# Kernel optimization log

Measured on AMD Instinct MI355X. Metric: run time of the kernel, lower is better.

## Reference

```python
import jax, jax.numpy as jnp
import numpy as np

N = 100000   # nodes
E = 1600000  # edges (avg degree 16)
IN = 128
HID = 128


def _glorot(key, shape):
    fan_in = shape[1]
    return jax.random.normal(key, shape, jnp.float32) * (1.0 / np.sqrt(fan_in))


def setup_inputs() -> dict:
    key = jax.random.key(0)
    ks = jax.random.split(key, 8)
    x = jax.random.normal(ks[0], (N, IN), jnp.float32)
    edge_index = jax.random.randint(ks[1], (2, E), 0, N, dtype=jnp.int64)
    return {
        "x": x,
        "edge_index": edge_index,
        "W1_l": _glorot(ks[2], (HID, IN)),
        "W1_r": _glorot(ks[3], (HID, IN)),
        "b1": jnp.zeros((HID,), jnp.float32),
        "W2_l": _glorot(ks[4], (HID, HID)),
        "W2_r": _glorot(ks[5], (HID, HID)),
        "b2": jnp.zeros((HID,), jnp.float32),
    }


def _sage_conv(x, src, dst, W_l, W_r, b):
    # message = x[src]; mean-aggregate onto dst; out = lin_l(mean) + lin_r(x) + b
    msg = x[src]                                                # [E, d]
    agg = jax.ops.segment_sum(msg, dst, num_segments=N)         # [N, d]
    cnt = jax.ops.segment_sum(jnp.ones((src.shape[0], 1), x.dtype), dst,
                              num_segments=N)                   # [N, 1]
    mean = agg / jnp.maximum(cnt, 1.0)
    return mean @ W_l.T + x @ W_r.T + b


def reference(x, edge_index, W1_l, W1_r, b1, W2_l, W2_r, b2):
    src, dst = edge_index[0], edge_index[1]
    h = jax.nn.relu(_sage_conv(x, src, dst, W1_l, W1_r, b1))
    return _sage_conv(h, src, dst, W2_l, W2_r, b2)
```

## Files before the change

kernel.cpp:

```cpp
#include <hip/hip_runtime.h>
#include <stdint.h>

#define N_NODES 100000
#define NE      1600000
#define DIM     128
#define NBUCKET 391

typedef __attribute__((ext_vector_type(8)))  __bf16 bf16x8;
typedef __attribute__((ext_vector_type(16))) float  f32x16;

#define ROW_B   0u
#define PART_B  401408u
#define BCUR_B  401920u
#define SRC_B   409600u
#define XB_B    6809600u
#define HB_B    32409600u
#define MB_B    58009600u
#define W1_B    83609600u
#define W2_B    83675136u
#define BPAIR_B 83740672u

#define SCAN_B 1024
#define SCAN_NB 98

__device__ __forceinline__ uint32_t f2b_rne(float f) {
    uint32_t u = __float_as_uint(f);
    return (u + 0x7FFFu + ((u >> 16) & 1u)) >> 16;
}
__device__ __forceinline__ float b2f_lo(uint32_t u) { return __uint_as_float(u << 16); }
__device__ __forceinline__ float b2f_hi(uint32_t u) { return __uint_as_float(u & 0xFFFF0000u); }

__global__ void k_hist(const int* __restrict__ dst, int* __restrict__ deg) {
    int e = blockIdx.x * 256 + threadIdx.x;
    if (e < NE) atomicAdd(&deg[dst[e]], 1);
}

__global__ __launch_bounds__(SCAN_B) void k_scan1(int* __restrict__ deg, int* __restrict__ part) {
    __shared__ int sm[SCAN_B];
    int tid = threadIdx.x;
    int i = blockIdx.x * SCAN_B + tid;
    int v = (i < N_NODES) ? deg[i] : 0;
    sm[tid] = v;
    __syncthreads();
    for (int off = 1; off < SCAN_B; off <<= 1) {
        int t = (tid >= off) ? sm[tid - off] : 0;
        __syncthreads();
        sm[tid] += t;
        __syncthreads();
    }
    if (i < N_NODES) deg[i] = sm[tid] - v;
    if (tid == SCAN_B - 1) part[blockIdx.x] = sm[tid];
}

__global__ __launch_bounds__(128) void k_scan2(int* __restrict__ part, int* __restrict__ rowptr) {
    __shared__ int sm[128];
    int tid = threadIdx.x;
    int v = (tid < SCAN_NB) ? part[tid] : 0;
    sm[tid] = v;
    __syncthreads();
    for (int off = 1; off < 128; off <<= 1) {
        int t = (tid >= off) ? sm[tid - off] : 0;
        __syncthreads();
        sm[tid] += t;
        __syncthreads();
    }
    if (tid < SCAN_NB) part[tid] = sm[tid] - v;
    if (tid == 0) rowptr[N_NODES] = NE;
}

__global__ __launch_bounds__(SCAN_B) void k_scan3(int* __restrict__ deg, const int* __restrict__ part) {
    int i = blockIdx.x * SCAN_B + threadIdx.x;
    if (i < N_NODES) deg[i] += part[blockIdx.x];
}

__global__ void k_binit(const int* __restrict__ rowptr, int* __restrict__ bcur) {
    int b = blockIdx.x * 256 + threadIdx.x;
    if (b < NBUCKET) bcur[b] = rowptr[b << 8];
}

#define BK_WG   512
#define BK_EPW  3125
__global__ __launch_bounds__(1024) void k_bucket(
    const int* __restrict__ src, const int* __restrict__ dst,
    int* __restrict__ bcur, int2* __restrict__ bpair) {
    __shared__ int hist[392];
    __shared__ int base[392];
    __shared__ int cur[392];
    const int tid = threadIdx.x;
    const int e0 = blockIdx.x * BK_EPW;
    const int e1 = e0 + BK_EPW;

    if (tid < 392) { hist[tid] = 0; cur[tid] = 0; }
    __syncthreads();
    for (int e = e0 + tid; e < e1; e += 1024)
        atomicAdd(&hist[dst[e] >> 8], 1);
    __syncthreads();
    if (tid < 392) {
        int h = hist[tid];
        base[tid] = h ? atomicAdd(&bcur[tid], h) : 0;
    }
    __syncthreads();
    for (int e = e0 + tid; e < e1; e += 1024) {
        int d = dst[e];
        int b = d >> 8;
        int loc = atomicAdd(&cur[b], 1);
        bpair[(size_t)(base[b] + loc)] = make_int2(src[e], d);
    }
}

__global__ __launch_bounds__(256) void k_sortb(
    const int* __restrict__ rowptr, const int2* __restrict__ bpair,
    int* __restrict__ ssrc) {
    __shared__ int cur[256];
    const int b = blockIdx.x;
    const int tid = threadIdx.x;
    const int n0 = b << 8;
    int idx = n0 + tid;
    cur[tid] = (idx < N_NODES) ? rowptr[idx] : NE;
    __syncthreads();
    const int bstart = rowptr[n0];
    const int bend = (b == NBUCKET - 1) ? NE : rowptr[n0 + 256];
    for (int e = bstart + tid; e < bend; e += 256) {
        int2 p = bpair[e];
        int slot = atomicAdd(&cur[p.y & 255], 1);
        ssrc[slot] = p.x;
    }
}

__global__ __launch_bounds__(256) void k_cvt_x(const float* __restrict__ x, uint32_t* __restrict__ xb) {
    size_t i = (size_t)blockIdx.x * 256 + threadIdx.x;
    if (i * 4 >= (size_t)N_NODES * DIM) return;
    float4 v = *reinterpret_cast<const float4*>(x + i * 4);
    uint2 o;
    o.x = f2b_rne(v.x) | (f2b_rne(v.y) << 16);
    o.y = f2b_rne(v.z) | (f2b_rne(v.w) << 16);
    *reinterpret_cast<uint2*>(xb + i * 2) = o;
}

__global__ __launch_bounds__(256) void k_cvt_w(
    const float* __restrict__ W1l, const float* __restrict__ W1r,
    const float* __restrict__ W2l, const float* __restrict__ W2r,
    uint16_t* __restrict__ w1, uint16_t* __restrict__ w2) {
    int gid = blockIdx.x * 256 + threadIdx.x;
    int layer = gid >> 13;
    int e = (gid & 8191) * 4;
    int row = e >> 8;
    int col = e & 255;
    const float* Wl = layer ? W2l : W1l;
    const float* Wr = layer ? W2r : W1r;
    const float* srcm = (col < 128) ? Wl : Wr;
    int c = col & 127;
    float4 v = *reinterpret_cast<const float4*>(&srcm[row * 128 + c]);
    uint2 o;
    o.x = f2b_rne(v.x) | (f2b_rne(v.y) << 16);
    o.y = f2b_rne(v.z) | (f2b_rne(v.w) << 16);
    uint16_t* wd = layer ? w2 : w1;
    *reinterpret_cast<uint2*>(&wd[row * 256 + col]) = o;
}

__global__ __launch_bounds__(256) void k_agg(const int* __restrict__ rowptr,
                                             const int* __restrict__ ssrc,
                                             const uint32_t* __restrict__ featb,
                                             uint32_t* __restrict__ meanb) {
    int node = (int)((blockIdx.x * 256 + threadIdx.x) >> 6);
    if (node >= N_NODES) return;
    int lane = threadIdx.x & 63;
    int start = rowptr[node];
    int end   = rowptr[node + 1];

    float ax0 = 0.f, ay0 = 0.f, ax1 = 0.f, ay1 = 0.f;
    float ax2 = 0.f, ay2 = 0.f, ax3 = 0.f, ay3 = 0.f;

    int e = start;
    for (; e + 8 <= end; e += 8) {
        int s0 = ssrc[e + 0], s1 = ssrc[e + 1], s2 = ssrc[e + 2], s3 = ssrc[e + 3];
        int s4 = ssrc[e + 4], s5 = ssrc[e + 5], s6 = ssrc[e + 6], s7 = ssrc[e + 7];
        uint32_t u0 = featb[(size_t)s0 * 64 + lane];
        uint32_t u1 = featb[(size_t)s1 * 64 + lane];
        uint32_t u2 = featb[(size_t)s2 * 64 + lane];
        uint32_t u3 = featb[(size_t)s3 * 64 + lane];
        uint32_t u4 = featb[(size_t)s4 * 64 + lane];
        uint32_t u5 = featb[(size_t)s5 * 64 + lane];
        uint32_t u6 = featb[(size_t)s6 * 64 + lane];
        uint32_t u7 = featb[(size_t)s7 * 64 + lane];
        ax0 += b2f_lo(u0); ay0 += b2f_hi(u0);
        ax1 += b2f_lo(u1); ay1 += b2f_hi(u1);
        ax2 += b2f_lo(u2); ay2 += b2f_hi(u2);
        ax3 += b2f_lo(u3); ay3 += b2f_hi(u3);
        ax0 += b2f_lo(u4); ay0 += b2f_hi(u4);
        ax1 += b2f_lo(u5); ay1 += b2f_hi(u5);
        ax2 += b2f_lo(u6); ay2 += b2f_hi(u6);
        ax3 += b2f_lo(u7); ay3 += b2f_hi(u7);
    }
    if (e + 4 <= end) {
        int s0 = ssrc[e + 0], s1 = ssrc[e + 1], s2 = ssrc[e + 2], s3 = ssrc[e + 3];
        uint32_t u0 = featb[(size_t)s0 * 64 + lane];
        uint32_t u1 = featb[(size_t)s1 * 64 + lane];
        uint32_t u2 = featb[(size_t)s2 * 64 + lane];
        uint32_t u3 = featb[(size_t)s3 * 64 + lane];
        ax0 += b2f_lo(u0); ay0 += b2f_hi(u0);
        ax1 += b2f_lo(u1); ay1 += b2f_hi(u1);
        ax2 += b2f_lo(u2); ay2 += b2f_hi(u2);
        ax3 += b2f_lo(u3); ay3 += b2f_hi(u3);
        e += 4;
    }
    for (; e < end; ++e) {
        int s = ssrc[e];
        uint32_t u = featb[(size_t)s * 64 + lane];
        ax0 += b2f_lo(u); ay0 += b2f_hi(u);
    }

    int cnt = end - start;
    float inv = cnt > 0 ? 1.0f / (float)cnt : 0.0f;
    float ax = ((ax0 + ax1) + (ax2 + ax3)) * inv;
    float ay = ((ay0 + ay1) + (ay2 + ay3)) * inv;
    meanb[(size_t)node * 64 + lane] = f2b_rne(ax) | (f2b_rne(ay) << 16);
}

template <bool RELU, bool BF16_OUT>
__global__ __launch_bounds__(256) void k_layer(
    const uint16_t* __restrict__ meanb, const uint16_t* __restrict__ xb,
    const uint16_t* __restrict__ wcat, const float* __restrict__ bias,
    void* __restrict__ outp)
{
    const int tid = threadIdx.x;
    const int lane = tid & 63;
    const int w = tid >> 6;
    const int wm = (w >> 1) * 64, wn = (w & 1) * 64;
    const int lrow = lane & 31, lk = (lane >> 5) * 8;
    const int base = blockIdx.x * 128;

    f32x16 acc00, acc01, acc10, acc11;
#pragma unroll
    for (int r = 0; r < 16; ++r) { acc00[r] = 0.f; acc01[r] = 0.f; acc10[r] = 0.f; acc11[r] = 0.f; }

    int r0 = base + wm + lrow;
    int r1 = r0 + 32;
    if (r0 > N_NODES - 1) r0 = N_NODES - 1;
    if (r1 > N_NODES - 1) r1 = N_NODES - 1;
    const uint16_t* a0m = meanb + (size_t)r0 * DIM + lk;
    const uint16_t* a1m = meanb + (size_t)r1 * DIM + lk;
    const uint16_t* a0x = xb   + (size_t)r0 * DIM + lk;
    const uint16_t* a1x = xb   + (size_t)r1 * DIM + lk;
    const uint16_t* b0p = wcat + (size_t)(wn + lrow) * 256 + lk;
    const uint16_t* b1p = wcat + (size_t)(wn + 32 + lrow) * 256 + lk;

#pragma unroll
    for (int ks = 0; ks < 16; ++ks) {
        const int klocal = (ks & 7) * 16;
        bf16x8 a0 = *reinterpret_cast<const bf16x8*>(((ks < 8) ? a0m : a0x) + klocal);
        bf16x8 a1 = *reinterpret_cast<const bf16x8*>(((ks < 8) ? a1m : a1x) + klocal);
        bf16x8 b0 = *reinterpret_cast<const bf16x8*>(b0p + ks * 16);
        bf16x8 b1 = *reinterpret_cast<const bf16x8*>(b1p + ks * 16);
        acc00 = __builtin_amdgcn_mfma_f32_32x32x16_bf16(a0, b0, acc00, 0, 0, 0);
        acc01 = __builtin_amdgcn_mfma_f32_32x32x16_bf16(a0, b1, acc01, 0, 0, 0);
        acc10 = __builtin_amdgcn_mfma_f32_32x32x16_bf16(a1, b0, acc10, 0, 0, 0);
        acc11 = __builtin_amdgcn_mfma_f32_32x32x16_bf16(a1, b1, acc11, 0, 0, 0);
    }

    const float bc0 = bias[wn + lrow];
    const float bc1 = bias[wn + 32 + lrow];
    const int hi4 = 4 * (lane >> 5);

#define STORE_TILE(ACC, MI, NI, BB)                                            \
    {                                                                          \
        const int colg = wn + (NI) * 32 + lrow;                                \
        _Pragma("unroll")                                                      \
        for (int r = 0; r < 16; ++r) {                                         \
            int rowg = base + wm + (MI) * 32 + (r & 3) + 8 * (r >> 2) + hi4;   \
            if (rowg < N_NODES) {                                              \
                float v = ACC[r] + (BB);                                       \
                if (RELU) v = fmaxf(v, 0.0f);                                  \
                if (BF16_OUT)                                                  \
                    ((uint16_t*)outp)[(size_t)rowg * DIM + colg] =             \
                        (uint16_t)f2b_rne(v);                                  \
                else                                                           \
                    ((float*)outp)[(size_t)rowg * DIM + colg] = v;             \
            }                                                                  \
        }                                                                      \
    }
    STORE_TILE(acc00, 0, 0, bc0)
    STORE_TILE(acc01, 0, 1, bc1)
    STORE_TILE(acc10, 1, 0, bc0)
    STORE_TILE(acc11, 1, 1, bc1)
#undef STORE_TILE
}

extern "C" void kernel_launch(void* const* d_in, const int* in_sizes, int n_in,
                              void* d_out, int out_size, void* d_ws, size_t ws_size,
                              hipStream_t stream) {
    const float* x   = (const float*)d_in[0];
    const int*   ei  = (const int*)d_in[1];
    const float* W1l = (const float*)d_in[2];
    const float* W1r = (const float*)d_in[3];
    const float* b1  = (const float*)d_in[4];
    const float* W2l = (const float*)d_in[5];
    const float* W2r = (const float*)d_in[6];
    const float* b2  = (const float*)d_in[7];
    const int* src = ei;
    const int* dst = ei + NE;

    char* wsb = (char*)d_ws;
    int*      rowptr  = (int*)(wsb + ROW_B);
    int*      part    = (int*)(wsb + PART_B);
    int*      bcur    = (int*)(wsb + BCUR_B);
    int*      ssrc    = (int*)(wsb + SRC_B);
    uint32_t* xb32    = (uint32_t*)(wsb + XB_B);
    uint16_t* xb16    = (uint16_t*)(wsb + XB_B);
    uint32_t* hb32    = (uint32_t*)(wsb + HB_B);
    uint16_t* hb16    = (uint16_t*)(wsb + HB_B);
    uint32_t* mb32    = (uint32_t*)(wsb + MB_B);
    uint16_t* mb16    = (uint16_t*)(wsb + MB_B);
    uint16_t* w1      = (uint16_t*)(wsb + W1_B);
    uint16_t* w2      = (uint16_t*)(wsb + W2_B);
    int2*     bpair   = (int2*)(wsb + BPAIR_B);
    float*    outf    = (float*)d_out;

    hipMemsetAsync(rowptr, 0, (N_NODES + 1) * sizeof(int), stream);

    const int eb = (NE + 255) / 256;
    k_hist <<<eb, 256, 0, stream>>>(dst, rowptr);
    k_scan1<<<SCAN_NB, SCAN_B, 0, stream>>>(rowptr, part);
    k_scan2<<<1, 128, 0, stream>>>(part, rowptr);
    k_scan3<<<SCAN_NB, SCAN_B, 0, stream>>>(rowptr, part);
    k_binit<<<2, 256, 0, stream>>>(rowptr, bcur);
    k_bucket<<<BK_WG, 1024, 0, stream>>>(src, dst, bcur, bpair);
    k_sortb<<<NBUCKET, 256, 0, stream>>>(rowptr, bpair, ssrc);

    k_cvt_x<<<12500, 256, 0, stream>>>(x, xb32);
    k_cvt_w<<<64, 256, 0, stream>>>(W1l, W1r, W2l, W2r, w1, w2);

    const int agg_blocks = N_NODES / 4;
    const int layer_blocks = (N_NODES + 127) / 128;

    k_agg<<<agg_blocks, 256, 0, stream>>>(rowptr, ssrc, xb32, mb32);
    k_layer<true, true><<<layer_blocks, 256, 0, stream>>>(mb16, xb16, w1, b1, (void*)hb16);

    k_agg<<<agg_blocks, 256, 0, stream>>>(rowptr, ssrc, hb32, mb32);
    k_layer<false, false><<<layer_blocks, 256, 0, stream>>>(mb16, hb16, w2, b2, (void*)outf);
}
```

Measured before the change: 435.1 us.

## Replace per-node global histogram and scans with bucket-level histogram and local scans

```diff
diff --git a/kernel.cpp b/kernel.cpp
--- a/kernel.cpp
+++ b/kernel.cpp
@@ -10,8 +10,9 @@
 typedef __attribute__((ext_vector_type(16))) float  f32x16;
 
 #define ROW_B   0u
-#define PART_B  401408u
-#define BCUR_B  401920u
+#define BHIST_B 401408u
+#define BBASE_B 403456u
+#define BCUR_B  405504u
 #define SRC_B   409600u
 #define XB_B    6809600u
 #define HB_B    32409600u
@@ -20,9 +21,6 @@
 #define W2_B    83675136u
 #define BPAIR_B 83740672u
 
-#define SCAN_B 1024
-#define SCAN_NB 98
-
 __device__ __forceinline__ uint32_t f2b_rne(float f) {
     uint32_t u = __float_as_uint(f);
     return (u + 0x7FFFu + ((u >> 16) & 1u)) >> 16;
@@ -30,56 +28,45 @@
 __device__ __forceinline__ float b2f_lo(uint32_t u) { return __uint_as_float(u << 16); }
 __device__ __forceinline__ float b2f_hi(uint32_t u) { return __uint_as_float(u & 0xFFFF0000u); }
 
-__global__ void k_hist(const int* __restrict__ dst, int* __restrict__ deg) {
-    int e = blockIdx.x * 256 + threadIdx.x;
-    if (e < NE) atomicAdd(&deg[dst[e]], 1);
-}
-
-__global__ __launch_bounds__(SCAN_B) void k_scan1(int* __restrict__ deg, int* __restrict__ part) {
-    __shared__ int sm[SCAN_B];
-    int tid = threadIdx.x;
-    int i = blockIdx.x * SCAN_B + tid;
-    int v = (i < N_NODES) ? deg[i] : 0;
+#define BK_WG   512
+#define BK_EPW  3125
+
+__global__ __launch_bounds__(1024) void k_bhist(const int* __restrict__ dst,
+                                                int* __restrict__ bhist) {
+    __shared__ int h[392];
+    const int tid = threadIdx.x;
+    if (tid < 392) h[tid] = 0;
+    __syncthreads();
+    const int e0 = blockIdx.x * BK_EPW;
+    const int e1 = e0 + BK_EPW;
+    for (int e = e0 + tid; e < e1; e += 1024)
+        atomicAdd(&h[dst[e] >> 8], 1);
+    __syncthreads();
+    if (tid < 392) {
+        int v = h[tid];
+        if (v) atomicAdd(&bhist[tid], v);
+    }
+}
+
+__global__ __launch_bounds__(512) void k_bscan(const int* __restrict__ bhist,
+                                               int* __restrict__ bbase,
+                                               int* __restrict__ bcur) {
+    __shared__ int sm[512];
+    const int tid = threadIdx.x;
+    int v = (tid < NBUCKET) ? bhist[tid] : 0;
     sm[tid] = v;
     __syncthreads();
-    for (int off = 1; off < SCAN_B; off <<= 1) {
+    for (int off = 1; off < 512; off <<= 1) {
         int t = (tid >= off) ? sm[tid - off] : 0;
         __syncthreads();
         sm[tid] += t;
         __syncthreads();
     }
-    if (i < N_NODES) deg[i] = sm[tid] - v;
-    if (tid == SCAN_B - 1) part[blockIdx.x] = sm[tid];
-}
-
-__global__ __launch_bounds__(128) void k_scan2(int* __restrict__ part, int* __restrict__ rowptr) {
-    __shared__ int sm[128];
-    int tid = threadIdx.x;
-    int v = (tid < SCAN_NB) ? part[tid] : 0;
-    sm[tid] = v;
-    __syncthreads();
-    for (int off = 1; off < 128; off <<= 1) {
-        int t = (tid >= off) ? sm[tid - off] : 0;
-        __syncthreads();
-        sm[tid] += t;
-        __syncthreads();
-    }
-    if (tid < SCAN_NB) part[tid] = sm[tid] - v;
-    if (tid == 0) rowptr[N_NODES] = NE;
-}
-
-__global__ __launch_bounds__(SCAN_B) void k_scan3(int* __restrict__ deg, const int* __restrict__ part) {
-    int i = blockIdx.x * SCAN_B + threadIdx.x;
-    if (i < N_NODES) deg[i] += part[blockIdx.x];
-}
-
-__global__ void k_binit(const int* __restrict__ rowptr, int* __restrict__ bcur) {
-    int b = blockIdx.x * 256 + threadIdx.x;
-    if (b < NBUCKET) bcur[b] = rowptr[b << 8];
-}
-
-#define BK_WG   512
-#define BK_EPW  3125
+    int ex = sm[tid] - v;
+    if (tid <= NBUCKET) bbase[tid] = ex;
+    if (tid < NBUCKET) bcur[tid] = ex;
+}
+
 __global__ __launch_bounds__(1024) void k_bucket(
     const int* __restrict__ src, const int* __restrict__ dst,
     int* __restrict__ bcur, int2* __restrict__ bpair) {
@@ -109,17 +96,36 @@
 }
 
 __global__ __launch_bounds__(256) void k_sortb(
-    const int* __restrict__ rowptr, const int2* __restrict__ bpair,
-    int* __restrict__ ssrc) {
+    const int* __restrict__ bbase, const int2* __restrict__ bpair,
+    int* __restrict__ rowptr, int* __restrict__ ssrc) {
+    __shared__ int deg[256];
+    __shared__ int sm[256];
     __shared__ int cur[256];
     const int b = blockIdx.x;
     const int tid = threadIdx.x;
     const int n0 = b << 8;
+    const int bstart = bbase[b];
+    const int bend   = bbase[b + 1];
+
+    deg[tid] = 0;
+    __syncthreads();
+    for (int e = bstart + tid; e < bend; e += 256)
+        atomicAdd(&deg[bpair[e].y & 255], 1);
+    __syncthreads();
+    int v = deg[tid];
+    sm[tid] = v;
+    __syncthreads();
+    for (int off = 1; off < 256; off <<= 1) {
+        int t = (tid >= off) ? sm[tid - off] : 0;
+        __syncthreads();
+        sm[tid] += t;
+        __syncthreads();
+    }
+    int ex = sm[tid] - v;
     int idx = n0 + tid;
-    cur[tid] = (idx < N_NODES) ? rowptr[idx] : NE;
-    __syncthreads();
-    const int bstart = rowptr[n0];
-    const int bend = (b == NBUCKET - 1) ? NE : rowptr[n0 + 256];
+    if (idx <= N_NODES) rowptr[idx] = bstart + ex;
+    cur[tid] = bstart + ex;
+    __syncthreads();
     for (int e = bstart + tid; e < bend; e += 256) {
         int2 p = bpair[e];
         int slot = atomicAdd(&cur[p.y & 255], 1);
@@ -302,7 +308,8 @@
 
     char* wsb = (char*)d_ws;
     int*      rowptr  = (int*)(wsb + ROW_B);
-    int*      part    = (int*)(wsb + PART_B);
+    int*      bhist   = (int*)(wsb + BHIST_B);
+    int*      bbase   = (int*)(wsb + BBASE_B);
     int*      bcur    = (int*)(wsb + BCUR_B);
     int*      ssrc    = (int*)(wsb + SRC_B);
     uint32_t* xb32    = (uint32_t*)(wsb + XB_B);
@@ -316,16 +323,12 @@
     int2*     bpair   = (int2*)(wsb + BPAIR_B);
     float*    outf    = (float*)d_out;
 
-    hipMemsetAsync(rowptr, 0, (N_NODES + 1) * sizeof(int), stream);
-
-    const int eb = (NE + 255) / 256;
-    k_hist <<<eb, 256, 0, stream>>>(dst, rowptr);
-    k_scan1<<<SCAN_NB, SCAN_B, 0, stream>>>(rowptr, part);
-    k_scan2<<<1, 128, 0, stream>>>(part, rowptr);
-    k_scan3<<<SCAN_NB, SCAN_B, 0, stream>>>(rowptr, part);
-    k_binit<<<2, 256, 0, stream>>>(rowptr, bcur);
+    hipMemsetAsync(bhist, 0, 392 * sizeof(int), stream);
+
+    k_bhist <<<BK_WG, 1024, 0, stream>>>(dst, bhist);
+    k_bscan <<<1, 512, 0, stream>>>(bhist, bbase, bcur);
     k_bucket<<<BK_WG, 1024, 0, stream>>>(src, dst, bcur, bpair);
-    k_sortb<<<NBUCKET, 256, 0, stream>>>(rowptr, bpair, ssrc);
+    k_sortb <<<NBUCKET, 256, 0, stream>>>(bbase, bpair, rowptr, ssrc);
 
     k_cvt_x<<<12500, 256, 0, stream>>>(x, xb32);
     k_cvt_w<<<64, 256, 0, stream>>>(W1l, W1r, W2l, W2r, w1, w2);
```

Result: faster. 380.3 us (-12.6%).
